# Performance work log

Hardware: AMD Instinct MI355X
Metric: run time of the kernel (lower is better)

## Reference

```python
import jax, jax.numpy as jnp
import numpy as np

N_HEAD = 16
N_EMBD = 2048
HEAD_DIM = N_EMBD // N_HEAD  # 128
B, T = 4, 2048
BASE_THETA = 10000.0


def _rotary_tables(seq_len, dim, dtype):
    inv_freq = 1.0 / (BASE_THETA ** (jnp.arange(0, dim, 2, dtype=jnp.float32) / dim))
    t = jnp.arange(seq_len, dtype=jnp.float32)
    freqs = jnp.outer(t, inv_freq)  # [T, dim/2]
    cos = jnp.cos(freqs)[None, :, None, :].astype(dtype)
    sin = jnp.sin(freqs)[None, :, None, :].astype(dtype)
    return cos, sin


def _apply_rotary(x, cos, sin):
    # x: [B, T, H, D]; rotate pairs (x[..., :D/2], x[..., D/2:])
    d = x.shape[3] // 2
    x1, x2 = x[..., :d], x[..., d:]
    y1 = x1 * cos + x2 * sin
    y2 = -x1 * sin + x2 * cos
    return jnp.concatenate([y1, y2], axis=3).astype(x.dtype)


def setup_inputs() -> dict:
    key = jax.random.key(0)
    ks = jax.random.split(key, 5)
    scale = 1.0 / np.sqrt(N_EMBD)
    return {
        "x": jax.random.normal(ks[0], (B, T, N_EMBD), dtype=jnp.float32),
        "wq": jax.random.normal(ks[1], (N_EMBD, N_EMBD), dtype=jnp.float32) * scale,
        "wk": jax.random.normal(ks[2], (N_EMBD, N_EMBD), dtype=jnp.float32) * scale,
        "wv": jax.random.normal(ks[3], (N_EMBD, N_EMBD), dtype=jnp.float32) * scale,
        "wo": jax.random.normal(ks[4], (N_EMBD, N_EMBD), dtype=jnp.float32) * scale,
    }


def reference(x, wq, wk, wv, wo):
    Bc, Tc, C = x.shape
    H, D = N_HEAD, HEAD_DIM
    # bias-free projections (nn.Linear applies x @ W.T)
    q = (x @ wq.T).reshape(Bc, Tc, H, D)
    k = (x @ wk.T).reshape(Bc, Tc, H, D)
    v = (x @ wv.T).reshape(Bc, Tc, H, D)
    cos, sin = _rotary_tables(Tc, D, x.dtype)
    # original module applies rotary TWICE (once before a dead SDPA, once after)
    q = _apply_rotary(_apply_rotary(q, cos, sin), cos, sin)
    k = _apply_rotary(_apply_rotary(k, cos, sin), cos, sin)
    # causal attention (flex_attention with causal block_mask, default scale)
    scores = jnp.einsum("bthd,bshd->bhts", q, k) / jnp.sqrt(jnp.asarray(D, x.dtype))
    causal = jnp.tril(jnp.ones((Tc, Tc), dtype=bool))
    scores = jnp.where(causal[None, None, :, :], scores, jnp.asarray(-jnp.inf, scores.dtype))
    attn = jax.nn.softmax(scores, axis=-1)
    y = jnp.einsum("bhts,bshd->bthd", attn, v).reshape(Bc, Tc, C)
    return y @ wo.T
```

## Files before the change

### kernel.cpp

```cpp
#include <hip/hip_runtime.h>
#include <math.h>

typedef unsigned short u16;
typedef __attribute__((ext_vector_type(4))) float f32x4;
typedef __attribute__((ext_vector_type(8))) __bf16 bf16x8;
typedef __attribute__((ext_vector_type(4))) unsigned short u16x4;
typedef __attribute__((ext_vector_type(8))) unsigned short u16x8;

#define GLL16(gp, lp) __builtin_amdgcn_global_load_lds( \
    (__attribute__((address_space(1))) void*)(void*)(gp), \
    (__attribute__((address_space(3))) void*)(void*)(lp), 16, 0, 0)

__device__ __forceinline__ u16 f2bf(float x) {
    unsigned u = __float_as_uint(x);
    return (u16)((u + 0x7FFFu + ((u >> 16) & 1u)) >> 16);
}
__device__ __forceinline__ float bf2f(u16 h) { return __uint_as_float(((unsigned)h) << 16); }

__device__ __forceinline__ f32x4 mfma16(bf16x8 a, bf16x8 b, f32x4 c) {
    return __builtin_amdgcn_mfma_f32_16x16x32_bf16(a, b, c, 0, 0, 0);
}

__global__ void cvt_f32_bf16(const float* __restrict__ s, u16* __restrict__ d, int n4) {
    int i = blockIdx.x * 256 + threadIdx.x;
    if (i < n4) {
        float4 v = ((const float4*)s)[i];
        u16x4 o = { f2bf(v.x), f2bf(v.y), f2bf(v.z), f2bf(v.w) };
        ((u16x4*)d)[i] = o;
    }
}

__global__ void rope_table_k(float2* __restrict__ tab) {
    int id = blockIdx.x * 256 + threadIdx.x;
    int t = id >> 6, j = id & 63;
    float freq = exp2f(-((float)(2 * j) / 128.f) * 13.287712379549449f);
    float ang = 2.f * (float)t * freq;
    float sv, cv;
    sincosf(ang, &sv, &cv);
    float2 r; r.x = cv; r.y = sv;
    tab[id] = r;
}

template <int MODE>
__global__ __launch_bounds__(512, 2) void gemm_nt(const u16* __restrict__ A, const u16* __restrict__ Bw,
                                                  u16* __restrict__ Qo, u16* __restrict__ Ko,
                                                  u16* __restrict__ Vt, float* __restrict__ Out,
                                                  const float2* __restrict__ tab, float qscale, int K) {
    extern __shared__ u16 smem[];
    const int tid = threadIdx.x;
    const int lane = tid & 63;
    const int qd = lane >> 4, ln = lane & 15;
    const int wid = tid >> 6;
    const int wr = wid >> 2, wc = wid & 3;

    constexpr int NBY = (MODE == 0) ? 24 : 8;
    const int id = (int)blockIdx.x;
    const int xcd = id & 7, slot = id >> 3;
    const int m0 = ((slot / NBY) * 8 + xcd) * 256;
    const int n0 = (slot % NBY) * 256;

    int sr[2], skc[2];
#pragma unroll
    for (int l = 0; l < 2; ++l) {
        const int i = l * 512 + tid;
        sr[l] = i >> 3;
        skc[l] = (i & 7) ^ (sr[l] & 7);
    }

    auto stage = [&](int tt, int hx) {
        const u16* gp = (hx < 2) ? A : Bw;
        const int x0 = (hx < 2) ? m0 : n0;
        const int h = hx & 1;
        u16* lb = &smem[(tt & 1) * 32768 + (hx >> 1) * 16384 + h * 8192];
#pragma unroll
        for (int l = 0; l < 2; ++l)
            GLL16(gp + (size_t)(x0 + 128 * h + sr[l]) * K + tt * 64 + skc[l] * 8,
                  &lb[(l * 512 + tid) * 8]);
    };

    f32x4 acc[8][4];
#pragma unroll
    for (int mi = 0; mi < 8; ++mi)
#pragma unroll
        for (int ni = 0; ni < 4; ++ni) acc[mi][ni] = f32x4{0.f, 0.f, 0.f, 0.f};

    const int arow = (wr * 128 + ln) * 64;
    const int brow = (wc * 64 + ln) * 64;
    const int cxk[2] = { (qd ^ (ln & 7)) * 8, ((qd + 4) ^ (ln & 7)) * 8 };

    const int niter = K >> 6;
    stage(0, 0); stage(0, 1); stage(0, 2); stage(0, 3);
    stage(1, 0);

#pragma unroll 2
    for (int t = 0; t < niter; ++t) {
        const u16* As = &smem[(t & 1) * 32768];
        const u16* Bs = As + 16384;
        const bool pf = (t + 1 < niter);
        if (pf) asm volatile("s_waitcnt vmcnt(2)" ::: "memory");
        else    asm volatile("s_waitcnt vmcnt(0)" ::: "memory");
        asm volatile("s_barrier" ::: "memory");
        bf16x8 a0[4][2], b0[2][2];
#pragma unroll
        for (int mi = 0; mi < 4; ++mi)
#pragma unroll
            for (int ks = 0; ks < 2; ++ks)
                a0[mi][ks] = *(const bf16x8*)&As[arow + mi * 1024 + cxk[ks]];
#pragma unroll
        for (int ni = 0; ni < 2; ++ni)
#pragma unroll
            for (int ks = 0; ks < 2; ++ks)
                b0[ni][ks] = *(const bf16x8*)&Bs[brow + ni * 1024 + cxk[ks]];
        if (pf) stage(t + 1, 1);
        __builtin_amdgcn_s_setprio(1);
#pragma unroll
        for (int mi = 0; mi < 4; ++mi)
#pragma unroll
            for (int ni = 0; ni < 2; ++ni)
#pragma unroll
                for (int ks = 0; ks < 2; ++ks)
                    acc[mi][ni] = mfma16(a0[mi][ks], b0[ni][ks], acc[mi][ni]);
        __builtin_amdgcn_s_setprio(0);
        asm volatile("s_barrier" ::: "memory");
        bf16x8 b1[2][2];
#pragma unroll
        for (int ni = 0; ni < 2; ++ni)
#pragma unroll
            for (int ks = 0; ks < 2; ++ks)
                b1[ni][ks] = *(const bf16x8*)&Bs[brow + (ni + 2) * 1024 + cxk[ks]];
        if (pf) stage(t + 1, 2);
        __builtin_amdgcn_s_setprio(1);
#pragma unroll
        for (int mi = 0; mi < 4; ++mi)
#pragma unroll
            for (int ni = 0; ni < 2; ++ni)
#pragma unroll
                for (int ks = 0; ks < 2; ++ks)
                    acc[mi][ni + 2] = mfma16(a0[mi][ks], b1[ni][ks], acc[mi][ni + 2]);
        __builtin_amdgcn_s_setprio(0);
        asm volatile("s_barrier" ::: "memory");
        bf16x8 a1[4][2];
#pragma unroll
        for (int mi = 0; mi < 4; ++mi)
#pragma unroll
            for (int ks = 0; ks < 2; ++ks)
                a1[mi][ks] = *(const bf16x8*)&As[arow + (mi + 4) * 1024 + cxk[ks]];
        if (pf) stage(t + 1, 3);
        __builtin_amdgcn_s_setprio(1);
#pragma unroll
        for (int mi = 0; mi < 4; ++mi)
#pragma unroll
            for (int ni = 0; ni < 2; ++ni)
#pragma unroll
                for (int ks = 0; ks < 2; ++ks)
                    acc[mi + 4][ni] = mfma16(a1[mi][ks], b0[ni][ks], acc[mi + 4][ni]);
        __builtin_amdgcn_s_setprio(0);
        asm volatile("s_barrier" ::: "memory");
        if (t + 2 < niter) stage(t + 2, 0);
        __builtin_amdgcn_s_setprio(1);
#pragma unroll
        for (int mi = 0; mi < 4; ++mi)
#pragma unroll
            for (int ni = 0; ni < 2; ++ni)
#pragma unroll
                for (int ks = 0; ks < 2; ++ks)
                    acc[mi + 4][ni + 2] = mfma16(a1[mi][ks], b1[ni][ks], acc[mi + 4][ni + 2]);
        __builtin_amdgcn_s_setprio(0);
    }
    __syncthreads();

    if constexpr (MODE == 0) {
        const int sec = n0 >> 11;
        if (sec <= 1) {
#pragma unroll
            for (int mi = 0; mi < 8; ++mi)
#pragma unroll
                for (int ni = 0; ni < 4; ++ni) {
                    const int col = wc * 64 + ni * 16 + ln;
                    const int cc = col >> 3, co = col & 7;
#pragma unroll
                    for (int r = 0; r < 4; ++r) {
                        const int row = wr * 128 + mi * 16 + qd * 4 + r;
                        smem[row * 256 + ((cc ^ (row & 15)) * 8) + co] = f2bf(acc[mi][ni][r]);
                    }
                }
            __syncthreads();
            const float qs = (sec == 0) ? qscale : 1.0f;
            u16* dstb = (sec == 0 ? Qo : Ko);
#pragma unroll
            for (int it = 0; it < 8; ++it) {
                const int c = it * 512 + tid;
                const int m = c >> 4, hh = (c >> 3) & 1, d8 = c & 7;
                const u16x8 lo = *(const u16x8*)&smem[m * 256 + (((hh * 16 + d8) ^ (m & 15)) * 8)];
                const u16x8 hi = *(const u16x8*)&smem[m * 256 + (((hh * 16 + 8 + d8) ^ (m & 15)) * 8)];
                const int t = (m0 + m) & 2047;
                const float2* tb = tab + t * 64 + d8 * 8;
                u16x8 o1, o2;
#pragma unroll
                for (int i = 0; i < 8; ++i) {
                    const float x1 = bf2f(lo[i]), x2 = bf2f(hi[i]);
                    const float2 cs = tb[i];
                    o1[i] = f2bf((x1 * cs.x + x2 * cs.y) * qs);
                    o2[i] = f2bf((x2 * cs.x - x1 * cs.y) * qs);
                }
                u16* dst = dstb + (size_t)(m0 + m) * 2048 + (n0 & 2047) + hh * 128 + d8 * 8;
                *(u16x8*)dst = o1;
                *(u16x8*)(dst + 64) = o2;
            }
        } else {
            const int bb = m0 >> 11;
#pragma unroll
            for (int mi = 0; mi < 8; ++mi) {
                const int mbase = wr * 128 + mi * 16 + qd * 4;
                const int mch = mbase >> 3, moff = mbase & 7;
#pragma unroll
                for (int ni = 0; ni < 4; ++ni) {
                    const int nl = wc * 64 + ni * 16 + ln;
                    u16x4 pk = { f2bf(acc[mi][ni][0]), f2bf(acc[mi][ni][1]),
                                 f2bf(acc[mi][ni][2]), f2bf(acc[mi][ni][3]) };
                    *(u16x4*)&smem[nl * 256 + ((mch ^ (nl & 15)) * 8) + moff] = pk;
                }
            }
            __syncthreads();
#pragma unroll
            for (int i = 0; i < 16; ++i) {
                const int c = i * 512 + tid;
                const int nl = c >> 5, ch = c & 31;
                const u16x8 v = *(const u16x8*)&smem[nl * 256 + ch * 8];
                const int mch = ch ^ (nl & 15);
                const int hd = (n0 - 4096) + nl;
                *(u16x8*)&Vt[((size_t)(bb * 2048 + hd)) * 2048 + (m0 & 2047) + mch * 8] = v;
            }
        }
    } else {
        const int mg0 = m0 + wr * 128 + qd * 4;
        const int ng0 = n0 + wc * 64 + ln;
#pragma unroll
        for (int mi = 0; mi < 8; ++mi)
#pragma unroll
            for (int ni = 0; ni < 4; ++ni) {
                const int ng = ng0 + ni * 16;
#pragma unroll
                for (int r = 0; r < 4; ++r)
                    Out[(size_t)(mg0 + mi * 16 + r) * 2048 + ng] = acc[mi][ni][r];
            }
    }
}

__global__ __launch_bounds__(512, 4) void attn_kernel(const u16* __restrict__ Qb, const u16* __restrict__ Kb,
                                                      const u16* __restrict__ Vt, u16* __restrict__ Yb) {
    extern __shared__ u16 smem[];
    u16* QP = smem;
    u16* KsB = smem + 8192;
    u16* VsB = smem + 8192 + 16384;

    const int tid = threadIdx.x;
    const int lane = tid & 63;
    const int qd = lane >> 4, ln = lane & 15;
    const int wid = tid >> 6;
    const int id = (int)blockIdx.x;
    const int px = id >> 6;
    const int bh = id & 63;
    const int b = bh >> 4, h = bh & 15;

    const u16* Qbh = Qb + ((size_t)b * 2048 * 16 + h) * 128;
    const u16* Kbh = Kb + ((size_t)b * 2048 * 16 + h) * 128;
    const u16* Vbh = Vt + ((size_t)(b * 16 + h) * 128) * 2048;

    int lC[2], kOff[2], vOff[2];
#pragma unroll
    for (int p = 0; p < 2; ++p) {
        const int c = p * 512 + tid;
        lC[p] = c * 8;
        { const int r = c >> 4, cc = (c & 15) ^ (r & 7); kOff[p] = r * 2048 + cc * 8; }
        { const int rv = c >> 3, cc = (c & 7) ^ (rv & 7); vOff[p] = rv * 2048 + cc * 8; }
    }

    bf16x8 onesf;
#pragma unroll
    for (int i = 0; i < 8; ++i) onesf[i] = (__bf16)1.0f;

    for (int half = 0; half < 2; ++half) {
        const int qt = half ? px : (15 - px);
        const int q0 = qt * 128;
        const int wq = q0 + wid * 16;
        const int nkt = 2 * qt + 2;

        __syncthreads();
#pragma unroll
        for (int p = 0; p < 2; ++p)
            GLL16(Qbh + (size_t)q0 * 2048 + kOff[p], &QP[lC[p]]);
        __syncthreads();
        bf16x8 qf[4];
        if (wid < 4) {
            const int lr = wid * 16 + ln;
#pragma unroll
            for (int ks = 0; ks < 4; ++ks)
                qf[ks] = *(const bf16x8*)&QP[lr * 128 + (((ks * 4 + qd) ^ (lr & 7)) * 8)];
        }
        __syncthreads();
#pragma unroll
        for (int p = 0; p < 2; ++p)
            GLL16(Qbh + (size_t)(q0 + 64) * 2048 + kOff[p], &QP[lC[p]]);
        __syncthreads();
        if (wid >= 4) {
            const int lr = (wid - 4) * 16 + ln;
#pragma unroll
            for (int ks = 0; ks < 4; ++ks)
                qf[ks] = *(const bf16x8*)&QP[lr * 128 + (((ks * 4 + qd) ^ (lr & 7)) * 8)];
        }
        __syncthreads();

#pragma unroll
        for (int p = 0; p < 2; ++p) GLL16(Kbh + kOff[p], &KsB[lC[p]]);
#pragma unroll
        for (int p = 0; p < 2; ++p) GLL16(Vbh + vOff[p], &VsB[lC[p]]);

        f32x4 o[8];
#pragma unroll
        for (int di = 0; di < 8; ++di) o[di] = f32x4{0.f, 0.f, 0.f, 0.f};
        f32x4 lacc = f32x4{0.f, 0.f, 0.f, 0.f};
        float Mr[4];
#pragma unroll
        for (int r = 0; r < 4; ++r) Mr[r] = -1e30f;

        for (int kt = 0; kt < nkt; ++kt) {
            const int k0 = kt * 64;
            asm volatile("s_barrier" ::: "memory");
            if (kt + 1 < nkt) {
                u16* kd = KsB + ((kt + 1) & 1) * 8192;
                u16* vd = VsB + ((kt + 1) & 1) * 8192;
#pragma unroll
                for (int p = 0; p < 2; ++p) GLL16(Kbh + (size_t)(k0 + 64) * 2048 + kOff[p], &kd[lC[p]]);
#pragma unroll
                for (int p = 0; p < 2; ++p) GLL16(Vbh + (size_t)(k0 + 64) + vOff[p], &vd[lC[p]]);
                asm volatile("s_waitcnt vmcnt(4)" ::: "memory");
            } else {
                asm volatile("s_waitcnt vmcnt(0)" ::: "memory");
            }
            asm volatile("s_barrier" ::: "memory");

            if (k0 <= wq + 15) {
                const u16* Kc = KsB + (kt & 1) * 8192;
                const u16* Vc = VsB + (kt & 1) * 8192;
                f32x4 s[4];
#pragma unroll
                for (int ni = 0; ni < 4; ++ni) s[ni] = f32x4{0.f, 0.f, 0.f, 0.f};
#pragma unroll
                for (int ks = 0; ks < 4; ++ks) {
                    bf16x8 kf[4];
#pragma unroll
                    for (int ni = 0; ni < 4; ++ni) {
                        const int row = ni * 16 + ln;
                        kf[ni] = *(const bf16x8*)&Kc[row * 128 + (((ks * 4 + qd) ^ (ln & 7)) * 8)];
                    }
#pragma unroll
                    for (int ni = 0; ni < 4; ++ni)
                        s[ni] = mfma16(qf[ks], kf[ni], s[ni]);
                }
                if (k0 + 63 > wq) {
#pragma unroll
                    for (int ni = 0; ni < 4; ++ni)
#pragma unroll
                        for (int r = 0; r < 4; ++r) {
                            const int qi = wq + qd * 4 + r;
                            const int ki = k0 + ni * 16 + ln;
                            if (ki > qi) s[ni][r] = -1e30f;
                        }
                }
                float rx[4];
#pragma unroll
                for (int r = 0; r < 4; ++r)
                    rx[r] = fmaxf(fmaxf(s[0][r], s[1][r]), fmaxf(s[2][r], s[3][r]));
#pragma unroll
                for (int st = 1; st < 16; st <<= 1)
#pragma unroll
                    for (int r = 0; r < 4; ++r)
                        rx[r] = fmaxf(rx[r], __shfl_xor(rx[r], st));
                float al[4];
                bool need = false;
#pragma unroll
                for (int r = 0; r < 4; ++r) {
                    const float nm = fmaxf(Mr[r], rx[r]);
                    al[r] = exp2f(Mr[r] - nm);
                    Mr[r] = nm;
                    need |= (al[r] != 1.0f);
                }
                if (__any(need)) {
#pragma unroll
                    for (int r = 0; r < 4; ++r) lacc[r] *= al[r];
#pragma unroll
                    for (int di = 0; di < 8; ++di)
#pragma unroll
                        for (int r = 0; r < 4; ++r) o[di][r] *= al[r];
                }
#pragma unroll
                for (int ni = 0; ni < 4; ++ni) {
                    const int cc0 = ni * 2 + (ln >> 3);
#pragma unroll
                    for (int r = 0; r < 4; ++r) {
                        const float p = exp2f(s[ni][r] - Mr[r]);
                        const int prow = wid * 16 + qd * 4 + r;
                        QP[prow * 64 + ((cc0 ^ ((prow >> 1) & 7)) * 8) + (ln & 7)] = f2bf(p);
                    }
                }
#pragma unroll
                for (int ks2 = 0; ks2 < 2; ++ks2) {
                    const int prow = wid * 16 + ln;
                    bf16x8 pf = *(const bf16x8*)&QP[prow * 64 + (((ks2 * 4 + qd) ^ ((prow >> 1) & 7)) * 8)];
                    lacc = mfma16(pf, onesf, lacc);
#pragma unroll
                    for (int di = 0; di < 8; ++di) {
                        const int row = di * 16 + ln;
                        bf16x8 vf = *(const bf16x8*)&Vc[row * 64 + (((ks2 * 4 + qd) ^ (ln & 7)) * 8)];
                        o[di] = mfma16(pf, vf, o[di]);
                    }
                }
            }
        }

        float inv[4];
#pragma unroll
        for (int r = 0; r < 4; ++r) inv[r] = 1.f / lacc[r];
#pragma unroll
        for (int di = 0; di < 8; ++di)
#pragma unroll
            for (int r = 0; r < 4; ++r) {
                const int t = q0 + wid * 16 + qd * 4 + r;
                const int d = di * 16 + ln;
                Yb[((size_t)((b * 2048 + t) * 16 + h)) * 128 + d] = f2bf(o[di][r] * inv[r]);
            }
    }
}

extern "C" void kernel_launch(void* const* d_in, const int* in_sizes, int n_in,
                              void* d_out, int out_size, void* d_ws, size_t ws_size,
                              hipStream_t stream) {
    const float* x  = (const float*)d_in[0];
    const float* wq = (const float*)d_in[1];
    const float* wk = (const float*)d_in[2];
    const float* wv = (const float*)d_in[3];
    const float* wo = (const float*)d_in[4];
    float* out = (float*)d_out;
    char* ws = (char*)d_ws;

    u16* xb     = (u16*)(ws);
    u16* wqkv   = (u16*)(ws + (size_t)33554432);
    u16* wob    = (u16*)(ws + (size_t)58720256);
    u16* Qb     = (u16*)(ws + (size_t)67108864);
    u16* Kb     = (u16*)(ws + (size_t)100663296);
    u16* Vt     = (u16*)(ws + (size_t)134217728);
    float2* tab = (float2*)(ws + (size_t)167772160);
    u16* Yb = xb;

    const float scl = 0.08838834764831845f * 1.4426950408889634f;

    cvt_f32_bf16<<<16384, 256, 0, stream>>>(x, xb, 4194304);
    cvt_f32_bf16<<<4096, 256, 0, stream>>>(wq, wqkv, 1048576);
    cvt_f32_bf16<<<4096, 256, 0, stream>>>(wk, wqkv + 4194304, 1048576);
    cvt_f32_bf16<<<4096, 256, 0, stream>>>(wv, wqkv + 8388608, 1048576);
    cvt_f32_bf16<<<4096, 256, 0, stream>>>(wo, wob, 1048576);
    rope_table_k<<<512, 256, 0, stream>>>(tab);

    hipFuncSetAttribute((const void*)gemm_nt<0>, hipFuncAttributeMaxDynamicSharedMemorySize, 131072);
    hipFuncSetAttribute((const void*)gemm_nt<1>, hipFuncAttributeMaxDynamicSharedMemorySize, 131072);

    gemm_nt<0><<<dim3(768), 512, 131072, stream>>>(xb, wqkv, Qb, Kb, Vt, nullptr, tab, scl, 2048);

    hipFuncSetAttribute((const void*)attn_kernel, hipFuncAttributeMaxDynamicSharedMemorySize, 81920);
    attn_kernel<<<dim3(512), 512, 81920, stream>>>(Qb, Kb, Vt, Yb);

    gemm_nt<1><<<dim3(256), 512, 131072, stream>>>(Yb, wob, nullptr, nullptr, nullptr, out, tab, 1.0f, 2048);
}
```

Before: 546.0 us.

## Restructure GEMM main loop into explicit two-stage ping-pong with finer-grained prefetch

Rewrites the bf16 GEMM K-loop as a manually unrolled pair of iterations that alternate between two fixed LDS buffers. Global-to-LDS loads for the next tiles are issued in quarter chunks between the MFMA clusters, and a barrier follows every cluster. Scheduling barriers are added after each barrier to stop the compiler from reordering instructions across it. The goal is better overlap of memory traffic with MFMA work and more predictable instruction interleaving, at the cost of twice as many barriers per iteration and more fragile vmcnt accounting.

Result: slower. 640.6 us (+17.3%).

```diff
diff --git a/kernel.cpp b/kernel.cpp
--- a/kernel.cpp
+++ b/kernel.cpp
@@ -88,85 +88,82 @@
     const int brow = (wc * 64 + ln) * 64;
     const int cxk[2] = { (qd ^ (ln & 7)) * 8, ((qd + 4) ^ (ln & 7)) * 8 };
 
+    auto rdA = [&](const u16* As, bf16x8 (&af)[4][2], int off) {
+#pragma unroll
+        for (int mi = 0; mi < 4; ++mi)
+#pragma unroll
+            for (int ks = 0; ks < 2; ++ks)
+                af[mi][ks] = *(const bf16x8*)&As[arow + (mi + off) * 1024 + cxk[ks]];
+    };
+    auto rdB = [&](const u16* Bs, bf16x8 (&bb)[2][2], int off) {
+#pragma unroll
+        for (int ni = 0; ni < 2; ++ni)
+#pragma unroll
+            for (int ks = 0; ks < 2; ++ks)
+                bb[ni][ks] = *(const bf16x8*)&Bs[brow + (ni + off) * 1024 + cxk[ks]];
+    };
+    auto clus = [&](bf16x8 (&af)[4][2], bf16x8 (&bb)[2][2], int mo, int no) {
+        __builtin_amdgcn_s_setprio(1);
+#pragma unroll
+        for (int mi = 0; mi < 4; ++mi)
+#pragma unroll
+            for (int ni = 0; ni < 2; ++ni)
+#pragma unroll
+                for (int ks = 0; ks < 2; ++ks)
+                    acc[mi + mo][ni + no] = mfma16(af[mi][ks], bb[ni][ks], acc[mi + mo][ni + no]);
+        __builtin_amdgcn_s_setprio(0);
+    };
+#define BARA do { asm volatile("s_barrier" ::: "memory"); __builtin_amdgcn_sched_barrier(0); } while (0)
+#define BARB asm volatile("s_barrier" ::: "memory")
+
     const int niter = K >> 6;
     stage(0, 0); stage(0, 1); stage(0, 2); stage(0, 3);
-    stage(1, 0);
-
-#pragma unroll 2
-    for (int t = 0; t < niter; ++t) {
-        const u16* As = &smem[(t & 1) * 32768];
-        const u16* Bs = As + 16384;
-        const bool pf = (t + 1 < niter);
-        if (pf) asm volatile("s_waitcnt vmcnt(2)" ::: "memory");
-        else    asm volatile("s_waitcnt vmcnt(0)" ::: "memory");
-        asm volatile("s_barrier" ::: "memory");
-        bf16x8 a0[4][2], b0[2][2];
-#pragma unroll
-        for (int mi = 0; mi < 4; ++mi)
-#pragma unroll
-            for (int ks = 0; ks < 2; ++ks)
-                a0[mi][ks] = *(const bf16x8*)&As[arow + mi * 1024 + cxk[ks]];
-#pragma unroll
-        for (int ni = 0; ni < 2; ++ni)
-#pragma unroll
-            for (int ks = 0; ks < 2; ++ks)
-                b0[ni][ks] = *(const bf16x8*)&Bs[brow + ni * 1024 + cxk[ks]];
-        if (pf) stage(t + 1, 1);
-        __builtin_amdgcn_s_setprio(1);
-#pragma unroll
-        for (int mi = 0; mi < 4; ++mi)
-#pragma unroll
-            for (int ni = 0; ni < 2; ++ni)
-#pragma unroll
-                for (int ks = 0; ks < 2; ++ks)
-                    acc[mi][ni] = mfma16(a0[mi][ks], b0[ni][ks], acc[mi][ni]);
-        __builtin_amdgcn_s_setprio(0);
-        asm volatile("s_barrier" ::: "memory");
-        bf16x8 b1[2][2];
-#pragma unroll
-        for (int ni = 0; ni < 2; ++ni)
-#pragma unroll
-            for (int ks = 0; ks < 2; ++ks)
-                b1[ni][ks] = *(const bf16x8*)&Bs[brow + (ni + 2) * 1024 + cxk[ks]];
-        if (pf) stage(t + 1, 2);
-        __builtin_amdgcn_s_setprio(1);
-#pragma unroll
-        for (int mi = 0; mi < 4; ++mi)
-#pragma unroll
-            for (int ni = 0; ni < 2; ++ni)
-#pragma unroll
-                for (int ks = 0; ks < 2; ++ks)
-                    acc[mi][ni + 2] = mfma16(a0[mi][ks], b1[ni][ks], acc[mi][ni + 2]);
-        __builtin_amdgcn_s_setprio(0);
-        asm volatile("s_barrier" ::: "memory");
-        bf16x8 a1[4][2];
-#pragma unroll
-        for (int mi = 0; mi < 4; ++mi)
-#pragma unroll
-            for (int ks = 0; ks < 2; ++ks)
-                a1[mi][ks] = *(const bf16x8*)&As[arow + (mi + 4) * 1024 + cxk[ks]];
-        if (pf) stage(t + 1, 3);
-        __builtin_amdgcn_s_setprio(1);
-#pragma unroll
-        for (int mi = 0; mi < 4; ++mi)
-#pragma unroll
-            for (int ni = 0; ni < 2; ++ni)
-#pragma unroll
-                for (int ks = 0; ks < 2; ++ks)
-                    acc[mi + 4][ni] = mfma16(a1[mi][ks], b0[ni][ks], acc[mi + 4][ni]);
-        __builtin_amdgcn_s_setprio(0);
-        asm volatile("s_barrier" ::: "memory");
-        if (t + 2 < niter) stage(t + 2, 0);
-        __builtin_amdgcn_s_setprio(1);
-#pragma unroll
-        for (int mi = 0; mi < 4; ++mi)
-#pragma unroll
-            for (int ni = 0; ni < 2; ++ni)
-#pragma unroll
-                for (int ks = 0; ks < 2; ++ks)
-                    acc[mi + 4][ni + 2] = mfma16(a1[mi][ks], b1[ni][ks], acc[mi + 4][ni + 2]);
-        __builtin_amdgcn_s_setprio(0);
-    }
+    stage(1, 2); stage(1, 3);
+    asm volatile("s_waitcnt vmcnt(4)" ::: "memory");
+    asm volatile("s_barrier" ::: "memory");
+
+    for (int i = 0; i < (niter >> 1); ++i) {
+        const int t0 = 2 * i, t1 = 2 * i + 1;
+        const u16* As0 = &smem[0];
+        const u16* Bs0 = &smem[16384];
+        const u16* As1 = &smem[32768];
+        const u16* Bs1 = &smem[49152];
+        const bool lastit = (i == (niter >> 1) - 1);
+        bf16x8 a0[4][2], a1[4][2], b0[2][2], b1[2][2];
+
+        rdA(As0, a0, 0); rdB(Bs0, b0, 0);
+        stage(t1, 0);
+        BARA; clus(a0, b0, 0, 0); BARB;
+        rdB(Bs0, b1, 2);
+        stage(t1, 1);
+        BARA; clus(a0, b1, 0, 2); BARB;
+        rdA(As0, a1, 4);
+        if (!lastit) stage(t0 + 2, 2);
+        BARA; clus(a1, b0, 4, 0); BARB;
+        if (!lastit) {
+            stage(t0 + 2, 3);
+            asm volatile("s_waitcnt vmcnt(4)" ::: "memory");
+        } else {
+            asm volatile("s_waitcnt vmcnt(0)" ::: "memory");
+        }
+        BARA; clus(a1, b1, 4, 2); BARB;
+        rdA(As1, a0, 0); rdB(Bs1, b0, 0);
+        if (!lastit) stage(t0 + 2, 0);
+        BARA; clus(a0, b0, 0, 0); BARB;
+        rdB(Bs1, b1, 2);
+        if (!lastit) stage(t0 + 2, 1);
+        BARA; clus(a0, b1, 0, 2); BARB;
+        rdA(As1, a1, 4);
+        if (!lastit) stage(t1 + 2, 2);
+        BARA; clus(a1, b0, 4, 0); BARB;
+        if (!lastit) {
+            stage(t1 + 2, 3);
+            asm volatile("s_waitcnt vmcnt(4)" ::: "memory");
+        }
+        BARA; clus(a1, b1, 4, 2); BARB;
+    }
+#undef BARA
+#undef BARB
     __syncthreads();
 
     if constexpr (MODE == 0) {
```

## Restructure GEMM mainloop to BK=32 with four-stage async LDS pipeline

Applied to the files above, without the earlier changes.

Halves the K-tile from 64 to 32 and replaces the double-buffered schedule (two buffers, four sub-stages per iteration) with a four-slot ring buffer that prefetches three tiles ahead. The LDS swizzle and fragment addressing are rebuilt for 32-wide rows, and each iteration now has two barrier-separated MFMA phases instead of four. The goal is deeper latency hiding of global loads at the same LDS footprint, at the cost of more loop iterations and a barrier per 16 MFMAs. Bank-conflict behaviour changes with the new swizzle.

After: 576.1 us. 1.06x slower.

```diff
diff --git a/kernel.cpp b/kernel.cpp
--- a/kernel.cpp
+++ b/kernel.cpp
@@ -63,18 +63,17 @@
 #pragma unroll
     for (int l = 0; l < 2; ++l) {
         const int i = l * 512 + tid;
-        sr[l] = i >> 3;
-        skc[l] = (i & 7) ^ (sr[l] & 7);
-    }
-
-    auto stage = [&](int tt, int hx) {
-        const u16* gp = (hx < 2) ? A : Bw;
-        const int x0 = (hx < 2) ? m0 : n0;
-        const int h = hx & 1;
-        u16* lb = &smem[(tt & 1) * 32768 + (hx >> 1) * 16384 + h * 8192];
+        sr[l] = i >> 2;
+        skc[l] = (i & 3) ^ ((sr[l] >> 1) & 3);
+    }
+
+    auto stage = [&](int tt, int w) {
+        const u16* gp = w ? Bw : A;
+        const int x0 = w ? n0 : m0;
+        u16* lb = &smem[(tt & 3) * 16384 + w * 8192];
 #pragma unroll
         for (int l = 0; l < 2; ++l)
-            GLL16(gp + (size_t)(x0 + 128 * h + sr[l]) * K + tt * 64 + skc[l] * 8,
+            GLL16(gp + (size_t)(x0 + sr[l]) * K + tt * 32 + skc[l] * 8,
                   &lb[(l * 512 + tid) * 8]);
     };
 
@@ -84,87 +83,46 @@
 #pragma unroll
         for (int ni = 0; ni < 4; ++ni) acc[mi][ni] = f32x4{0.f, 0.f, 0.f, 0.f};
 
-    const int arow = (wr * 128 + ln) * 64;
-    const int brow = (wc * 64 + ln) * 64;
-    const int cxk[2] = { (qd ^ (ln & 7)) * 8, ((qd + 4) ^ (ln & 7)) * 8 };
-
-    const int niter = K >> 6;
-    stage(0, 0); stage(0, 1); stage(0, 2); stage(0, 3);
-    stage(1, 0);
-
-#pragma unroll 2
+    const int arow = (wr * 128 + ln) * 32;
+    const int brow = (wc * 64 + ln) * 32;
+    const int cx = (qd ^ ((ln >> 1) & 3)) * 8;
+
+    const int niter = K >> 5;
+    stage(0, 0); stage(0, 1);
+    stage(1, 0); stage(1, 1);
+    stage(2, 0); stage(2, 1);
+
     for (int t = 0; t < niter; ++t) {
-        const u16* As = &smem[(t & 1) * 32768];
-        const u16* Bs = As + 16384;
-        const bool pf = (t + 1 < niter);
-        if (pf) asm volatile("s_waitcnt vmcnt(2)" ::: "memory");
-        else    asm volatile("s_waitcnt vmcnt(0)" ::: "memory");
+        const u16* As = &smem[(t & 3) * 16384];
+        const u16* Bs = As + 8192;
+        if (t < niter - 2)       asm volatile("s_waitcnt vmcnt(8)" ::: "memory");
+        else if (t == niter - 2) asm volatile("s_waitcnt vmcnt(4)" ::: "memory");
+        else                     asm volatile("s_waitcnt vmcnt(0)" ::: "memory");
         asm volatile("s_barrier" ::: "memory");
-        bf16x8 a0[4][2], b0[2][2];
+        bf16x8 a[4], b[4];
+#pragma unroll
+        for (int mi = 0; mi < 4; ++mi) a[mi] = *(const bf16x8*)&As[arow + mi * 512 + cx];
+#pragma unroll
+        for (int ni = 0; ni < 4; ++ni) b[ni] = *(const bf16x8*)&Bs[brow + ni * 512 + cx];
+        if (t + 3 < niter) stage(t + 3, 0);
+        __builtin_amdgcn_s_setprio(1);
 #pragma unroll
         for (int mi = 0; mi < 4; ++mi)
 #pragma unroll
-            for (int ks = 0; ks < 2; ++ks)
-                a0[mi][ks] = *(const bf16x8*)&As[arow + mi * 1024 + cxk[ks]];
-#pragma unroll
-        for (int ni = 0; ni < 2; ++ni)
-#pragma unroll
-            for (int ks = 0; ks < 2; ++ks)
-                b0[ni][ks] = *(const bf16x8*)&Bs[brow + ni * 1024 + cxk[ks]];
-        if (pf) stage(t + 1, 1);
-        __builtin_amdgcn_s_setprio(1);
-#pragma unroll
-        for (int mi = 0; mi < 4; ++mi)
-#pragma unroll
-            for (int ni = 0; ni < 2; ++ni)
-#pragma unroll
-                for (int ks = 0; ks < 2; ++ks)
-                    acc[mi][ni] = mfma16(a0[mi][ks], b0[ni][ks], acc[mi][ni]);
+            for (int ni = 0; ni < 4; ++ni)
+                acc[mi][ni] = mfma16(a[mi], b[ni], acc[mi][ni]);
         __builtin_amdgcn_s_setprio(0);
         asm volatile("s_barrier" ::: "memory");
-        bf16x8 b1[2][2];
-#pragma unroll
-        for (int ni = 0; ni < 2; ++ni)
-#pragma unroll
-            for (int ks = 0; ks < 2; ++ks)
-                b1[ni][ks] = *(const bf16x8*)&Bs[brow + (ni + 2) * 1024 + cxk[ks]];
-        if (pf) stage(t + 1, 2);
+        bf16x8 a2[4];
+#pragma unroll
+        for (int mi = 0; mi < 4; ++mi) a2[mi] = *(const bf16x8*)&As[arow + (mi + 4) * 512 + cx];
+        if (t + 3 < niter) stage(t + 3, 1);
         __builtin_amdgcn_s_setprio(1);
 #pragma unroll
         for (int mi = 0; mi < 4; ++mi)
 #pragma unroll
-            for (int ni = 0; ni < 2; ++ni)
-#pragma unroll
-                for (int ks = 0; ks < 2; ++ks)
-                    acc[mi][ni + 2] = mfma16(a0[mi][ks], b1[ni][ks], acc[mi][ni + 2]);
-        __builtin_amdgcn_s_setprio(0);
-        asm volatile("s_barrier" ::: "memory");
-        bf16x8 a1[4][2];
-#pragma unroll
-        for (int mi = 0; mi < 4; ++mi)
-#pragma unroll
-            for (int ks = 0; ks < 2; ++ks)
-                a1[mi][ks] = *(const bf16x8*)&As[arow + (mi + 4) * 1024 + cxk[ks]];
-        if (pf) stage(t + 1, 3);
-        __builtin_amdgcn_s_setprio(1);
-#pragma unroll
-        for (int mi = 0; mi < 4; ++mi)
-#pragma unroll
-            for (int ni = 0; ni < 2; ++ni)
-#pragma unroll
-                for (int ks = 0; ks < 2; ++ks)
-                    acc[mi + 4][ni] = mfma16(a1[mi][ks], b0[ni][ks], acc[mi + 4][ni]);
-        __builtin_amdgcn_s_setprio(0);
-        asm volatile("s_barrier" ::: "memory");
-        if (t + 2 < niter) stage(t + 2, 0);
-        __builtin_amdgcn_s_setprio(1);
-#pragma unroll
-        for (int mi = 0; mi < 4; ++mi)
-#pragma unroll
-            for (int ni = 0; ni < 2; ++ni)
-#pragma unroll
-                for (int ks = 0; ks < 2; ++ks)
-                    acc[mi + 4][ni + 2] = mfma16(a1[mi][ks], b1[ni][ks], acc[mi + 4][ni + 2]);
+            for (int ni = 0; ni < 4; ++ni)
+                acc[mi + 4][ni] = mfma16(a2[mi], b[ni], acc[mi + 4][ni]);
         __builtin_amdgcn_s_setprio(0);
     }
     __syncthreads();
```
